# Kernel optimization log

Measured on AMD Instinct MI355X. Metric: run time of the kernel, lower is better.

The kernel has to match this reference:

```python
import jax, jax.numpy as jnp
import numpy as np

B, N, E, H = 4, 1024, 1024, 16
D = E // H

def setup_inputs() -> dict:
    key = jax.random.key(0)
    ks = jax.random.split(key, 5)
    return {
        "x": jax.random.normal(ks[0], (B, N, E), dtype=jnp.float32),
        "Wqkv": jax.random.normal(ks[1], (E, 3 * E), dtype=jnp.float32) * 0.02,
        "bqkv": jax.random.normal(ks[2], (3 * E,), dtype=jnp.float32) * 0.02,
        "Wfc": jax.random.normal(ks[3], (E, E), dtype=jnp.float32) * 0.02,
        "bfc": jax.random.normal(ks[4], (E,), dtype=jnp.float32) * 0.02,
    }

def reference(x, Wqkv, bqkv, Wfc, bfc):
    b, n, e = x.shape
    h, d = H, E // H
    qkv = x @ Wqkv + bqkv                      # [b, n, 3e]
    q, k, v = jnp.split(qkv, 3, axis=-1)       # each [b, n, e]
    # view to [b, n, h, d] then RAW reshape to [b, h, n, d] (faithful to original,
    # which uses .reshape, not transpose — mixes seq/head axes)
    q = q.reshape(b, n, h, d).reshape(b, h, n, d)
    k = k.reshape(b, n, h, d).reshape(b, h, n, d)
    v = v.reshape(b, n, h, d).reshape(b, h, n, d)
    scores = jnp.einsum('bhqd,bhkd->bhqk', q, k) / jnp.sqrt(jnp.float32(d))
    causal = jnp.triu(jnp.ones((n, n), dtype=bool), k=1)  # True above diagonal
    scores = jnp.where(causal, -jnp.inf, scores)
    attn = jax.nn.softmax(scores, axis=-1)
    out = jnp.einsum('bhqk,bhkd->bhqd', attn, v)          # [b, h, n, d]
    # raw reshape back to [b, n, h, d] then flatten heads (faithful)
    out = out.reshape(b, n, h, d).reshape(b, n, e)
    return out @ Wfc + bfc
```

## Files before the change

kernel.cpp:

```cpp
#include <hip/hip_runtime.h>


typedef __bf16 bf16x8 __attribute__((ext_vector_type(8)));
typedef float f32x4 __attribute__((ext_vector_type(4)));

__device__ __forceinline__ unsigned short f2bf(float f) {
    unsigned u = __float_as_uint(f);
    u += 0x7fffu + ((u >> 16) & 1u);
    return (unsigned short)(u >> 16);
}

union FragU { uint4 u; bf16x8 v; };

__device__ __forceinline__ bf16x8 ld_frag(const unsigned short* p) {
    FragU x; x.u = *(const uint4*)p; return x.v;
}

__device__ __forceinline__ void gload_lds16(const void* g, void* l) {
    __builtin_amdgcn_global_load_lds(
        (const __attribute__((address_space(1))) void*)g,
        (__attribute__((address_space(3))) void*)l, 16, 0, 0);
}

__global__ void cvt_bf16(const float* __restrict__ in, unsigned short* __restrict__ out, int n4) {
    int i = blockIdx.x * blockDim.x + threadIdx.x;
    int stride = gridDim.x * blockDim.x;
    for (; i < n4; i += stride) {
        float4 f = ((const float4*)in)[i];
        unsigned a = (unsigned)f2bf(f.x) | ((unsigned)f2bf(f.y) << 16);
        unsigned b = (unsigned)f2bf(f.z) | ((unsigned)f2bf(f.w) << 16);
        ((uint2*)out)[i] = make_uint2(a, b);
    }
}

__global__ void transpose_cvt(const float* __restrict__ W, unsigned short* __restrict__ Wt,
                              int rows, int cols) {
    __shared__ float tile[32][33];
    int c0 = blockIdx.x * 32, r0 = blockIdx.y * 32;
    for (int i = threadIdx.y; i < 32; i += 8)
        tile[i][threadIdx.x] = W[(r0 + i) * cols + c0 + threadIdx.x];
    __syncthreads();
    for (int i = threadIdx.y; i < 32; i += 8)
        Wt[(c0 + i) * (long)rows + r0 + threadIdx.x] = f2bf(tile[threadIdx.x][i]);
}

__global__ void transpose_v(const unsigned short* __restrict__ v,
                            unsigned short* __restrict__ vt) {
    __shared__ unsigned short tile[32][33];
    int bh = blockIdx.z;
    int n0 = blockIdx.x * 32, d0 = blockIdx.y * 32;
    const unsigned short* src = v + (long)bh * 65536;
    unsigned short* dst = vt + (long)bh * 65536;
    for (int i = threadIdx.y; i < 32; i += 8)
        tile[i][threadIdx.x] = src[(n0 + i) * 64 + d0 + threadIdx.x];
    __syncthreads();
    for (int i = threadIdx.y; i < 32; i += 8)
        dst[(d0 + i) * 1024 + n0 + threadIdx.x] = tile[threadIdx.x][i];
}

template <int MODE>
__global__ __launch_bounds__(256) void gemm128(
    const unsigned short* __restrict__ A,
    const unsigned short* __restrict__ Bt,
    const float* __restrict__ bias,
    unsigned short* __restrict__ qb,
    unsigned short* __restrict__ kb,
    unsigned short* __restrict__ vb,
    float* __restrict__ outf)
{
    const int K = 1024;
    __shared__ unsigned short As[2][4096];
    __shared__ unsigned short Bs[2][4096];
    int t = threadIdx.x, lane = t & 63, w = t >> 6;
    int wm = w >> 1, wn = w & 1;
    int lrow = lane >> 4, lcol = lane & 15;
    int tn0 = blockIdx.x * 128, tm0 = blockIdx.y * 128;

    int seg0 = w * 1024;
    int seg1 = (w + 4) * 1024;
    int off0 = seg0 + lane * 16, off1 = seg1 + lane * 16;
    int r0 = off0 >> 6, cb0 = off0 & 63;
    int r1 = off1 >> 6, cb1 = off1 & 63;

    const char* gA = (const char*)A;
    const char* gB = (const char*)Bt;

    f32x4 acc[4][4] = {};

    auto STAGE = [&](int buf, int kt) {
        long kby = (long)kt * 2;
        gload_lds16(gA + (long)(tm0 + r0) * 2048 + kby + cb0, (char*)&As[buf][0] + seg0);
        gload_lds16(gA + (long)(tm0 + r1) * 2048 + kby + cb1, (char*)&As[buf][0] + seg1);
        gload_lds16(gB + (long)(tn0 + r0) * 2048 + kby + cb0, (char*)&Bs[buf][0] + seg0);
        gload_lds16(gB + (long)(tn0 + r1) * 2048 + kby + cb1, (char*)&Bs[buf][0] + seg1);
    };

    STAGE(0, 0);
    asm volatile("s_waitcnt vmcnt(0)");
    __syncthreads();

    int cur = 0;
    for (int kt = 0; kt < K; kt += 32) {
        if (kt + 32 < K) STAGE(cur ^ 1, kt + 32);

        bf16x8 af[4], bfr[4];
        #pragma unroll
        for (int mi = 0; mi < 4; ++mi)
            af[mi] = ld_frag(&As[cur][0] + (wm * 64 + mi * 16 + lcol) * 32 + lrow * 8);
        #pragma unroll
        for (int ni = 0; ni < 4; ++ni)
            bfr[ni] = ld_frag(&Bs[cur][0] + (wn * 64 + ni * 16 + lcol) * 32 + lrow * 8);
        #pragma unroll
        for (int mi = 0; mi < 4; ++mi)
            #pragma unroll
            for (int ni = 0; ni < 4; ++ni)
                acc[mi][ni] = __builtin_amdgcn_mfma_f32_16x16x32_bf16(af[mi], bfr[ni], acc[mi][ni], 0, 0, 0);

        __syncthreads();
        cur ^= 1;
    }

    #pragma unroll
    for (int mi = 0; mi < 4; ++mi) {
        int gr0 = tm0 + wm * 64 + mi * 16 + lrow * 4;
        #pragma unroll
        for (int ni = 0; ni < 4; ++ni) {
            int gc = tn0 + wn * 64 + ni * 16 + lcol;
            float bv = bias[gc];
            if (MODE == 0) {
                int sec = gc >> 10, ei = gc & 1023;
                unsigned short* dst = sec == 0 ? qb : (sec == 1 ? kb : vb);
                #pragma unroll
                for (int r = 0; r < 4; ++r)
                    dst[(long)(gr0 + r) * 1024 + ei] = f2bf(acc[mi][ni][r] + bv);
            } else {
                #pragma unroll
                for (int r = 0; r < 4; ++r)
                    outf[(long)(gr0 + r) * 1024 + gc] = acc[mi][ni][r] + bv;
            }
        }
    }
}

__global__ __launch_bounds__(256) void attn(
    const unsigned short* __restrict__ qbuf,
    const unsigned short* __restrict__ kbuf,
    const unsigned short* __restrict__ vtbuf,
    unsigned short* __restrict__ obuf)
{
    __shared__ char smem[4 * 32 * 68 * 4 + 512 + 512] __attribute__((aligned(16)));
    unsigned short (*Ps)[32][40] = (unsigned short (*)[32][40])smem;
    float* accS = (float*)smem;
    float* mS = (float*)(smem + 4 * 32 * 68 * 4);
    float* lS = mS + 128;

    int id = blockIdx.x;
    int xcd = id & 7, slot = id >> 3;
    int bh = xcd + 8 * (slot >> 4);
    int j = slot & 15;

    const unsigned short* Q  = qbuf + (long)bh * 65536;
    const unsigned short* Kp = kbuf + (long)bh * 65536;
    const unsigned short* VT = vtbuf + (long)bh * 65536;
    unsigned short* O = obuf + (long)bh * 65536;
    int t = threadIdx.x, lane = t & 63, w = t >> 6;
    int lrow = lane >> 4, lcol = lane & 15;
    const float NEG = -__builtin_inff();

    #pragma unroll
    for (int pass = 0; pass < 2; ++pass) {
        int qt = pass == 0 ? j : 31 - j;
        int qbase = qt * 32;
        int T = qt + 1;

        bf16x8 qf[2][2];
        #pragma unroll
        for (int qg = 0; qg < 2; ++qg)
            #pragma unroll
            for (int kc = 0; kc < 2; ++kc)
                qf[qg][kc] = ld_frag(Q + (long)(qbase + qg * 16 + lcol) * 64 + kc * 32 + lrow * 8);

        f32x4 acc[2][4] = {};
        float m_i[2] = {NEG, NEG}, l_i[2] = {0.f, 0.f};

        if (w < T) {
            int kt = w * 32;
            bf16x8 kf[2][2];
            #pragma unroll
            for (int kg = 0; kg < 2; ++kg)
                #pragma unroll
                for (int kc = 0; kc < 2; ++kc)
                    kf[kg][kc] = ld_frag(Kp + (long)(kt + kg * 16 + lcol) * 64 + kc * 32 + lrow * 8);

            for (;; kt += 128) {
                f32x4 s[2][2] = {};
                __builtin_amdgcn_s_setprio(1);
                #pragma unroll
                for (int kg = 0; kg < 2; ++kg)
                    #pragma unroll
                    for (int kc = 0; kc < 2; ++kc) {
                        s[0][kg] = __builtin_amdgcn_mfma_f32_16x16x32_bf16(kf[kg][kc], qf[0][kc], s[0][kg], 0, 0, 0);
                        s[1][kg] = __builtin_amdgcn_mfma_f32_16x16x32_bf16(kf[kg][kc], qf[1][kc], s[1][kg], 0, 0, 0);
                    }
                __builtin_amdgcn_s_setprio(0);

                bool more = kt + 128 < T * 32;
                bf16x8 kn[2][2];
                if (more) {
                    #pragma unroll
                    for (int kg = 0; kg < 2; ++kg)
                        #pragma unroll
                        for (int kc = 0; kc < 2; ++kc)
                            kn[kg][kc] = ld_frag(Kp + (long)(kt + 128 + kg * 16 + lcol) * 64 + kc * 32 + lrow * 8);
                }
                bf16x8 vf[4];
                #pragma unroll
                for (int dg = 0; dg < 4; ++dg)
                    vf[dg] = ld_frag(VT + (long)(dg * 16 + lcol) * 1024 + kt + lrow * 8);

                float tv[2][8], pmax[2];
                #pragma unroll
                for (int qg = 0; qg < 2; ++qg) {
                    int q = qbase + qg * 16 + lcol;
                    float mx = NEG;
                    #pragma unroll
                    for (int kg = 0; kg < 2; ++kg)
                        #pragma unroll
                        for (int r = 0; r < 4; ++r) {
                            int kglob = kt + kg * 16 + lrow * 4 + r;
                            float v = s[qg][kg][r] * 0.125f;
                            tv[qg][kg * 4 + r] = kglob > q ? NEG : v;
                            mx = fmaxf(mx, tv[qg][kg * 4 + r]);
                        }
                    mx = fmaxf(mx, __shfl_xor(mx, 16));
                    mx = fmaxf(mx, __shfl_xor(mx, 32));
                    pmax[qg] = mx;
                }
                float alpha[2] = {1.f, 1.f};
                bool small = (pmax[0] - m_i[0] <= 8.f) && (pmax[1] - m_i[1] <= 8.f);
                if (!__all(small)) {
                    #pragma unroll
                    for (int qg = 0; qg < 2; ++qg) {
                        float mnew = fmaxf(m_i[qg], pmax[qg]);
                        alpha[qg] = __expf(m_i[qg] - mnew);
                        m_i[qg] = mnew;
                    }
                    #pragma unroll
                    for (int qg = 0; qg < 2; ++qg)
                        #pragma unroll
                        for (int dg = 0; dg < 4; ++dg)
                            #pragma unroll
                            for (int r = 0; r < 4; ++r)
                                acc[qg][dg][r] *= alpha[qg];
                }
                #pragma unroll
                for (int qg = 0; qg < 2; ++qg) {
                    float p[8], ps = 0.f;
                    #pragma unroll
                    for (int jj = 0; jj < 8; ++jj) { p[jj] = __expf(tv[qg][jj] - m_i[qg]); ps += p[jj]; }
                    #pragma unroll
                    for (int kg = 0; kg < 2; ++kg) {
                        ushort4 pk;
                        pk.x = f2bf(p[kg * 4 + 0]); pk.y = f2bf(p[kg * 4 + 1]);
                        pk.z = f2bf(p[kg * 4 + 2]); pk.w = f2bf(p[kg * 4 + 3]);
                        *(ushort4*)&Ps[w][qg * 16 + lcol][kg * 16 + lrow * 4] = pk;
                    }
                    ps += __shfl_xor(ps, 16);
                    ps += __shfl_xor(ps, 32);
                    l_i[qg] = l_i[qg] * alpha[qg] + ps;
                }

                bf16x8 pb[2];
                pb[0] = ld_frag(&Ps[w][lcol][lrow * 8]);
                pb[1] = ld_frag(&Ps[w][16 + lcol][lrow * 8]);
                __builtin_amdgcn_s_setprio(1);
                #pragma unroll
                for (int dg = 0; dg < 4; ++dg) {
                    acc[0][dg] = __builtin_amdgcn_mfma_f32_16x16x32_bf16(vf[dg], pb[0], acc[0][dg], 0, 0, 0);
                    acc[1][dg] = __builtin_amdgcn_mfma_f32_16x16x32_bf16(vf[dg], pb[1], acc[1][dg], 0, 0, 0);
                }
                __builtin_amdgcn_s_setprio(0);

                if (!more) break;
                #pragma unroll
                for (int kg = 0; kg < 2; ++kg)
                    #pragma unroll
                    for (int kc = 0; kc < 2; ++kc)
                        kf[kg][kc] = kn[kg][kc];
            }
        }

        __syncthreads();
        #pragma unroll
        for (int qg = 0; qg < 2; ++qg) {
            int q = qg * 16 + lcol;
            if (lrow == 0) { mS[w * 32 + q] = m_i[qg]; lS[w * 32 + q] = l_i[qg]; }
            #pragma unroll
            for (int dg = 0; dg < 4; ++dg)
                *(f32x4*)&accS[(w * 32 + q) * 68 + dg * 16 + lrow * 4] = acc[qg][dg];
        }
        __syncthreads();

        {
            int qq = t >> 3, d0 = (t & 7) * 8;
            float m0 = mS[qq], m1 = mS[32 + qq], m2 = mS[64 + qq], m3 = mS[96 + qq];
            float M = fmaxf(fmaxf(m0, m1), fmaxf(m2, m3));
            float e0 = __expf(m0 - M), e1 = __expf(m1 - M), e2 = __expf(m2 - M), e3 = __expf(m3 - M);
            float L = e0 * lS[qq] + e1 * lS[32 + qq] + e2 * lS[64 + qq] + e3 * lS[96 + qq];
            float inv = 1.f / L;
            const float* a0 = &accS[qq * 68 + d0];
            const float* a1 = &accS[(32 + qq) * 68 + d0];
            const float* a2 = &accS[(64 + qq) * 68 + d0];
            const float* a3 = &accS[(96 + qq) * 68 + d0];
            unsigned short h[8];
            #pragma unroll
            for (int jj = 0; jj < 8; ++jj)
                h[jj] = f2bf((e0 * a0[jj] + e1 * a1[jj] + e2 * a2[jj] + e3 * a3[jj]) * inv);
            uint4 pk;
            pk.x = (unsigned)h[0] | ((unsigned)h[1] << 16);
            pk.y = (unsigned)h[2] | ((unsigned)h[3] << 16);
            pk.z = (unsigned)h[4] | ((unsigned)h[5] << 16);
            pk.w = (unsigned)h[6] | ((unsigned)h[7] << 16);
            *(uint4*)&O[(long)(qbase + qq) * 64 + d0] = pk;
        }
        __syncthreads();
    }
}

extern "C" void kernel_launch(void* const* d_in, const int* in_sizes, int n_in,
                              void* d_out, int out_size, void* d_ws, size_t ws_size,
                              hipStream_t stream) {
    const float* x    = (const float*)d_in[0];
    const float* Wqkv = (const float*)d_in[1];
    const float* bqkv = (const float*)d_in[2];
    const float* Wfc  = (const float*)d_in[3];
    const float* bfc  = (const float*)d_in[4];
    float* out = (float*)d_out;

    unsigned short* ws    = (unsigned short*)d_ws;
    unsigned short* xb    = ws;
    unsigned short* wqkvT = xb + (4u << 20);
    unsigned short* wfcT  = wqkvT + (3u << 20);
    unsigned short* qb    = wfcT + (1u << 20);
    unsigned short* kb    = qb + (4u << 20);
    unsigned short* vb    = kb + (4u << 20);
    unsigned short* vbT   = xb;
    unsigned short* ob    = vb;

    cvt_bf16<<<dim3(2048), dim3(256), 0, stream>>>(x, xb, (4 << 20) / 4);
    transpose_cvt<<<dim3(3072 / 32, 1024 / 32), dim3(32, 8), 0, stream>>>(Wqkv, wqkvT, 1024, 3072);
    transpose_cvt<<<dim3(1024 / 32, 1024 / 32), dim3(32, 8), 0, stream>>>(Wfc, wfcT, 1024, 1024);

    gemm128<0><<<dim3(24, 32), dim3(256), 0, stream>>>(xb, wqkvT, bqkv, qb, kb, vb, nullptr);
    transpose_v<<<dim3(32, 2, 64), dim3(32, 8), 0, stream>>>(vb, vbT);
    attn<<<dim3(1024), dim3(256), 0, stream>>>(qb, kb, vbT, ob);
    gemm128<1><<<dim3(8, 32), dim3(256), 0, stream>>>(ob, wfcT, bfc, nullptr, nullptr, nullptr, out);
}
```

Before: 120.9 us.

## Fold softmax scale into Q, use exp2, defer max reduction, packed bf16 cvt

Pre-scales Q by log2(e)/sqrt(d) in the QKV GEMM epilogue so the attention loop drops the per-score multiply and can use exp2 directly. Causal masking now runs only on the diagonal tile, and the cross-lane max shuffles are done only when some lane's local max exceeds the running max by more than a threshold. The bf16 packing of P uses the hardware v_cvt_pk_bf16_f32 instruction. The trade-off is slightly different rounding (Q is rounded after scaling) and a looser deferred-rescale bound that allows larger exponent values before rescaling.

```diff
diff --git a/kernel.cpp b/kernel.cpp
--- a/kernel.cpp
+++ b/kernel.cpp
@@ -3,11 +3,20 @@
 
 typedef __bf16 bf16x8 __attribute__((ext_vector_type(8)));
 typedef float f32x4 __attribute__((ext_vector_type(4)));
+
+#define QSCALE 0.18033688011112042f
+#define DEFER_THR 11.0f
 
 __device__ __forceinline__ unsigned short f2bf(float f) {
     unsigned u = __float_as_uint(f);
     u += 0x7fffu + ((u >> 16) & 1u);
     return (unsigned short)(u >> 16);
+}
+
+__device__ __forceinline__ unsigned cvtpk_bf16(float lo, float hi) {
+    unsigned r;
+    asm("v_cvt_pk_bf16_f32 %0, %1, %2" : "=v"(r) : "v"(lo), "v"(hi));
+    return r;
 }
 
 union FragU { uint4 u; bf16x8 v; };
@@ -130,9 +139,15 @@
             if (MODE == 0) {
                 int sec = gc >> 10, ei = gc & 1023;
                 unsigned short* dst = sec == 0 ? qb : (sec == 1 ? kb : vb);
-                #pragma unroll
-                for (int r = 0; r < 4; ++r)
-                    dst[(long)(gr0 + r) * 1024 + ei] = f2bf(acc[mi][ni][r] + bv);
+                if (sec == 0) {
+                    #pragma unroll
+                    for (int r = 0; r < 4; ++r)
+                        dst[(long)(gr0 + r) * 1024 + ei] = f2bf((acc[mi][ni][r] + bv) * QSCALE);
+                } else {
+                    #pragma unroll
+                    for (int r = 0; r < 4; ++r)
+                        dst[(long)(gr0 + r) * 1024 + ei] = f2bf(acc[mi][ni][r] + bv);
+                }
             } else {
                 #pragma unroll
                 for (int r = 0; r < 4; ++r)
@@ -218,56 +233,60 @@
                 for (int dg = 0; dg < 4; ++dg)
                     vf[dg] = ld_frag(VT + (long)(dg * 16 + lcol) * 1024 + kt + lrow * 8);
 
-                float tv[2][8], pmax[2];
+                float tv[2][8], lmax[2];
+                bool diag = (kt == qbase);
                 #pragma unroll
                 for (int qg = 0; qg < 2; ++qg) {
-                    int q = qbase + qg * 16 + lcol;
-                    float mx = NEG;
                     #pragma unroll
                     for (int kg = 0; kg < 2; ++kg)
                         #pragma unroll
-                        for (int r = 0; r < 4; ++r) {
-                            int kglob = kt + kg * 16 + lrow * 4 + r;
-                            float v = s[qg][kg][r] * 0.125f;
-                            tv[qg][kg * 4 + r] = kglob > q ? NEG : v;
-                            mx = fmaxf(mx, tv[qg][kg * 4 + r]);
-                        }
-                    mx = fmaxf(mx, __shfl_xor(mx, 16));
-                    mx = fmaxf(mx, __shfl_xor(mx, 32));
-                    pmax[qg] = mx;
-                }
-                float alpha[2] = {1.f, 1.f};
-                bool small = (pmax[0] - m_i[0] <= 8.f) && (pmax[1] - m_i[1] <= 8.f);
-                if (!__all(small)) {
+                        for (int r = 0; r < 4; ++r)
+                            tv[qg][kg * 4 + r] = s[qg][kg][r];
+                    if (diag) {
+                        #pragma unroll
+                        for (int kg = 0; kg < 2; ++kg)
+                            #pragma unroll
+                            for (int r = 0; r < 4; ++r)
+                                if (kg * 16 + lrow * 4 + r > qg * 16 + lcol)
+                                    tv[qg][kg * 4 + r] = NEG;
+                    }
+                    float a0 = fmaxf(tv[qg][0], tv[qg][1]), a1 = fmaxf(tv[qg][2], tv[qg][3]);
+                    float a2 = fmaxf(tv[qg][4], tv[qg][5]), a3 = fmaxf(tv[qg][6], tv[qg][7]);
+                    lmax[qg] = fmaxf(fmaxf(a0, a1), fmaxf(a2, a3));
+                }
+
+                bool ok = (lmax[0] <= m_i[0] + DEFER_THR) && (lmax[1] <= m_i[1] + DEFER_THR);
+                if (!__all(ok)) {
                     #pragma unroll
                     for (int qg = 0; qg < 2; ++qg) {
-                        float mnew = fmaxf(m_i[qg], pmax[qg]);
-                        alpha[qg] = __expf(m_i[qg] - mnew);
+                        float mx = fmaxf(lmax[qg], __shfl_xor(lmax[qg], 16));
+                        mx = fmaxf(mx, __shfl_xor(mx, 32));
+                        float mnew = fmaxf(m_i[qg], mx);
+                        float alpha = exp2f(m_i[qg] - mnew);
                         m_i[qg] = mnew;
-                    }
-                    #pragma unroll
-                    for (int qg = 0; qg < 2; ++qg)
+                        l_i[qg] *= alpha;
                         #pragma unroll
                         for (int dg = 0; dg < 4; ++dg)
                             #pragma unroll
                             for (int r = 0; r < 4; ++r)
-                                acc[qg][dg][r] *= alpha[qg];
-                }
+                                acc[qg][dg][r] *= alpha;
+                    }
+                }
+
                 #pragma unroll
                 for (int qg = 0; qg < 2; ++qg) {
                     float p[8], ps = 0.f;
                     #pragma unroll
-                    for (int jj = 0; jj < 8; ++jj) { p[jj] = __expf(tv[qg][jj] - m_i[qg]); ps += p[jj]; }
-                    #pragma unroll
-                    for (int kg = 0; kg < 2; ++kg) {
-                        ushort4 pk;
-                        pk.x = f2bf(p[kg * 4 + 0]); pk.y = f2bf(p[kg * 4 + 1]);
-                        pk.z = f2bf(p[kg * 4 + 2]); pk.w = f2bf(p[kg * 4 + 3]);
-                        *(ushort4*)&Ps[w][qg * 16 + lcol][kg * 16 + lrow * 4] = pk;
-                    }
+                    for (int jj = 0; jj < 8; ++jj) { p[jj] = exp2f(tv[qg][jj] - m_i[qg]); ps += p[jj]; }
+                    unsigned u0 = cvtpk_bf16(p[0], p[1]);
+                    unsigned u1 = cvtpk_bf16(p[2], p[3]);
+                    unsigned u2 = cvtpk_bf16(p[4], p[5]);
+                    unsigned u3 = cvtpk_bf16(p[6], p[7]);
+                    *(uint2*)&Ps[w][qg * 16 + lcol][lrow * 4]      = make_uint2(u0, u1);
+                    *(uint2*)&Ps[w][qg * 16 + lcol][16 + lrow * 4] = make_uint2(u2, u3);
                     ps += __shfl_xor(ps, 16);
                     ps += __shfl_xor(ps, 32);
-                    l_i[qg] = l_i[qg] * alpha[qg] + ps;
+                    l_i[qg] += ps;
                 }
 
                 bf16x8 pb[2];
@@ -305,7 +324,7 @@
             int qq = t >> 3, d0 = (t & 7) * 8;
             float m0 = mS[qq], m1 = mS[32 + qq], m2 = mS[64 + qq], m3 = mS[96 + qq];
             float M = fmaxf(fmaxf(m0, m1), fmaxf(m2, m3));
-            float e0 = __expf(m0 - M), e1 = __expf(m1 - M), e2 = __expf(m2 - M), e3 = __expf(m3 - M);
+            float e0 = exp2f(m0 - M), e1 = exp2f(m1 - M), e2 = exp2f(m2 - M), e3 = exp2f(m3 - M);
             float L = e0 * lS[qq] + e1 * lS[32 + qq] + e2 * lS[64 + qq] + e3 * lS[96 + qq];
             float inv = 1.f / L;
             const float* a0 = &accS[qq * 68 + d0];
```

After: 123.4 us. 2.1% more time.
